# Optimization experiments

Hardware: AMD Instinct MI355X
Metric: run time of the kernel (lower is better)

The kernel has to match this reference:

```python
import jax, jax.numpy as jnp
import numpy as np
from jax import lax

DN = ('NCHW', 'OIHW', 'NCHW')


def conv3x3(x, w, groups=1):
    return lax.conv_general_dilated(x, w, window_strides=(1, 1),
                                    padding=((1, 1), (1, 1)),
                                    dimension_numbers=DN,
                                    feature_group_count=groups)


def conv1x1(x, w):
    return lax.conv_general_dilated(x, w, window_strides=(1, 1),
                                    padding=((0, 0), (0, 0)),
                                    dimension_numbers=DN)


def l2_normalize(t, eps=1e-12):
    n = jnp.sqrt(jnp.sum(t * t, axis=-1, keepdims=True))
    return t / jnp.maximum(n, eps)


def setup_inputs() -> dict:
    key = jax.random.key(0)
    ks = jax.random.split(key, 10)
    B, C, H, W = 4, 64, 256, 256
    heads = 8
    s = 0.05
    return {
        'x': jax.random.normal(ks[0], (B, C, H, W), jnp.float32),
        'w_iem': jax.random.normal(ks[1], (C, C, 3, 3), jnp.float32) * s,
        'w_nem': jax.random.normal(ks[2], (C, C, 3, 3), jnp.float32) * s,
        'w_iem_dw': jax.random.normal(ks[3], (C, 1, 3, 3), jnp.float32) * s,
        'w_nem_dw': jax.random.normal(ks[4], (C, 1, 3, 3), jnp.float32) * s,
        'w_q': jax.random.normal(ks[5], (C, C, 1, 1), jnp.float32) * s,
        'w_k': jax.random.normal(ks[6], (C, C, 1, 1), jnp.float32) * s,
        'w_v': jax.random.normal(ks[7], (C, C, 1, 1), jnp.float32) * s,
        'w_proj': jax.random.normal(ks[8], (C, C, 1, 1), jnp.float32) * s,
        'temperature': jnp.ones((1, heads, 1, 1, 1, 1), jnp.float32),
    }


def igam_forward(x, w_iem, w_nem, w_iem_dw, w_nem_dw, w_q, w_k, w_v, w_proj,
                 temperature, num_heads=8, window_size=8):
    b, c, h, w = x.shape
    ws = window_size
    pad_h = (ws - h % ws) % ws
    pad_w = (ws - w % ws) % ws
    if pad_h or pad_w:  # replicate pad on right/bottom (static)
        x = jnp.pad(x, ((0, 0), (0, 0), (0, pad_h), (0, pad_w)), mode='edge')
    hp, wp = x.shape[-2:]
    heads = num_heads
    d = c // heads
    nh, nw = hp // ws, wp // ws

    illumination_map = conv3x3(jax.nn.sigmoid(conv3x3(x, w_iem)), w_iem_dw, groups=c)
    noise_map = conv3x3(jax.nn.sigmoid(conv3x3(x, w_nem)), w_nem_dw, groups=c)
    illum_scalar = jnp.mean(illumination_map, axis=1, keepdims=True)  # (b,1,hp,wp)
    noise_scalar = jnp.mean(noise_map, axis=1, keepdims=True)

    q = conv1x1(illumination_map, w_q)
    k = conv1x1(noise_map, w_k)
    v = conv1x1(x, w_v)

    def to_windows(t):  # (b,c,hp,wp) -> (b,heads,nh,nw,ws*ws,d)
        t = t.reshape(b, heads, d, hp, wp).transpose(0, 1, 3, 4, 2)
        t = t.reshape(b, heads, nh, ws, nw, ws, d).transpose(0, 1, 2, 4, 3, 5, 6)
        return t.reshape(b, heads, nh, nw, ws * ws, d)

    def scalar_to_windows(t):  # (b,1,hp,wp) -> (b,1,nh,nw,ws*ws,1)
        t = t.reshape(b, 1, nh, ws, nw, ws).transpose(0, 1, 2, 4, 3, 5)
        return t.reshape(b, 1, nh, nw, ws * ws, 1)

    qw = l2_normalize(to_windows(q)) * (1.0 + scalar_to_windows(illum_scalar))
    kw = l2_normalize(to_windows(k)) * jnp.clip(1.0 - scalar_to_windows(noise_scalar), 0.0, 1.0)
    vw = to_windows(v)

    scale = d ** (-0.5)
    attn = jnp.einsum('bhnmqd,bhnmkd->bhnmqk', qw, kw) * scale * temperature
    attn = jax.nn.softmax(attn, axis=-1)
    outw = jnp.einsum('bhnmqk,bhnmkd->bhnmqd', attn, vw)

    # merge windows back to (b, c, hp, wp)
    outw = outw.reshape(b, heads, nh, nw, ws, ws, d).transpose(0, 1, 6, 2, 4, 3, 5)
    out = outw.reshape(b, heads * d, nh * ws, nw * ws)
    if pad_h or pad_w:
        out = out[:, :, :h, :w]
    return conv1x1(out, w_proj)


def reference(x, w_iem, w_nem, w_iem_dw, w_nem_dw, w_q, w_k, w_v, w_proj,
              temperature):
    return igam_forward(x, w_iem, w_nem, w_iem_dw, w_nem_dw, w_q, w_k, w_v,
                        w_proj, temperature)
```

## Files before the change

kernel.cpp:

```cpp
#include <hip/hip_runtime.h>
#include <math.h>

#define W_ 256
#define H_ 256
#define HW 65536
#define CC 64

typedef _Float16 h16;
typedef _Float16 half8 __attribute__((ext_vector_type(8)));
typedef float f32x4  __attribute__((ext_vector_type(4)));
typedef float f32x16 __attribute__((ext_vector_type(16)));

__device__ __forceinline__ unsigned pk2(float a, float b) {
  union { h16 h[2]; unsigned u; } c;
  c.h[0] = (h16)a; c.h[1] = (h16)b;
  return c.u;
}
__device__ __forceinline__ void plswap(unsigned &a, unsigned &b) {
  asm volatile("v_permlane32_swap_b32 %0, %1" : "+v"(a), "+v"(b));
}

__global__ __launch_bounds__(256) void k_wprep(
    const float* __restrict__ wi, const float* __restrict__ wn, h16* __restrict__ Bt)
{
  int i = blockIdx.x * 256 + threadIdx.x;
  if (i >= 128 * 576) return;
  int co = i / 576, k = i - co * 576;
  int tap = k >> 6, ci = k & 63;
  const float* src = (co < 64) ? wi : wn;
  int c = co & 63;
  Bt[i] = (h16)src[(c * 64 + ci) * 9 + tap];
}

__global__ __launch_bounds__(256) void k_wprep2(
    const float* __restrict__ wq, const float* __restrict__ wk,
    const float* __restrict__ wv, const float* __restrict__ wp,
    const float* __restrict__ wdw1, const float* __restrict__ wdw2,
    h16* __restrict__ W)
{
  int i = blockIdx.x * 256 + threadIdx.x;
  if (i >= 17536) return;
  if (i < 16384) {
    int m = i >> 12, e = i & 4095;
    const float* s = (m == 0) ? wq : (m == 1) ? wk : (m == 2) ? wv : wp;
    W[i] = (h16)s[e];
  } else {
    int e = i - 16384;
    int pass = e / 576, rem = e - pass * 576;
    int tap = rem >> 6, c = rem & 63;
    const float* s = pass ? wdw2 : wdw1;
    W[i] = (h16)s[c * 9 + tap];
  }
}

__global__ __launch_bounds__(256) void k_xpose(
    const float* __restrict__ x, h16* __restrict__ xT)
{
  __shared__ __align__(16) char sm[64 * 132];
  const int tid = threadIdx.x;
  const int xt = blockIdx.x, y = blockIdx.y, b = blockIdx.z;
  const int x0 = xt * 64;
  const float* xb = x + ((size_t)b * CC) * HW + y * W_ + x0;
  const int ci = tid >> 2, q = tid & 3;
#pragma unroll
  for (int k = 0; k < 4; ++k) {
    const int pc = q + k * 4;
    float4 v = *(const float4*)(xb + (size_t)ci * HW + pc * 4);
    const int px = pc * 4;
    *(h16*)(sm + (px + 0) * 132 + ci * 2) = (h16)v.x;
    *(h16*)(sm + (px + 1) * 132 + ci * 2) = (h16)v.y;
    *(h16*)(sm + (px + 2) * 132 + ci * 2) = (h16)v.z;
    *(h16*)(sm + (px + 3) * 132 + ci * 2) = (h16)v.w;
  }
  __syncthreads();
  h16* dst = xT + (((size_t)b * 256 + y) * 256 + x0) * 64;
#pragma unroll
  for (int it = 0; it < 2; ++it) {
    int task = tid + it * 256;
    int px = task >> 3, c8 = task & 7;
    int4 d = *(const int4*)(sm + px * 132 + c8 * 16);
    *(int4*)(dst + px * 64 + c8 * 8) = d;
  }
}

__global__ __launch_bounds__(512) void k_conv3x3x2(
    const h16* __restrict__ xT, const h16* __restrict__ Bt,
    h16* __restrict__ T1, h16* __restrict__ T2)
{
  __shared__ __align__(16) char lds[38016];

  const int tid = threadIdx.x;
  const int b = blockIdx.z, ry = blockIdx.y, cx = blockIdx.x;
  const int y0 = ry * 2, x0 = cx * 64;

  {
    const h16* xb = xT + ((size_t)b * 256) * 256 * 64;
    int4 zero4; zero4.x = zero4.y = zero4.z = zero4.w = 0;
#pragma unroll
    for (int it = 0; it < 5; ++it) {
      int idx = tid + it * 512;
      if (idx < 2112) {
        int pxr = idx >> 3, c8 = idx & 7;
        int r = pxr / 66, c = pxr - r * 66;
        int gy = y0 - 1 + r, gx = x0 - 1 + c;
        int4 d = zero4;
        if ((unsigned)gy < 256u && (unsigned)gx < 256u)
          d = *(const int4*)(xb + ((size_t)(gy * 256 + gx)) * 64 + c8 * 8);
        *(int4*)(lds + pxr * 144 + c8 * 16) = d;
      }
    }
  }
  __syncthreads();

  const int wv = tid >> 6, lane = tid & 63;
  const int wn_ = wv & 3;
  const int wm_ = wv >> 2;
  const int cob = wn_ * 32;
  const int pxb = wm_ * 64;
  const int lg = lane >> 4, lr = lane & 15;

  const char* pB[4];
#pragma unroll
  for (int pi = 0; pi < 4; ++pi) {
    int opx = (pxb + pi * 16 + lr) & 63;
    pB[pi] = lds + (wm_ * 66 + opx) * 144 + lg * 16;
  }
  const h16* wb0 = Bt + (size_t)(cob + lr) * 576 + lg * 8;
  const h16* wb1 = wb0 + 16 * 576;

  f32x4 acc[2][4];
#pragma unroll
  for (int i = 0; i < 2; ++i)
#pragma unroll
    for (int j = 0; j < 4; ++j) acc[i][j] = (f32x4){0.f, 0.f, 0.f, 0.f};

#pragma unroll
  for (int tap = 0; tap < 9; ++tap) {
    const int dy = tap / 3, dx = tap - dy * 3;
#pragma unroll
    for (int kh = 0; kh < 2; ++kh) {
      const int loff = (dy * 66 + dx) * 144 + kh * 64;
      const int koff = tap * 64 + kh * 32;
      half8 a0 = *(const half8*)(wb0 + koff);
      half8 a1 = *(const half8*)(wb1 + koff);
      half8 b0 = *(const half8*)(pB[0] + loff);
      half8 b1 = *(const half8*)(pB[1] + loff);
      half8 b2 = *(const half8*)(pB[2] + loff);
      half8 b3 = *(const half8*)(pB[3] + loff);
      acc[0][0] = __builtin_amdgcn_mfma_f32_16x16x32_f16(a0, b0, acc[0][0], 0, 0, 0);
      acc[0][1] = __builtin_amdgcn_mfma_f32_16x16x32_f16(a0, b1, acc[0][1], 0, 0, 0);
      acc[0][2] = __builtin_amdgcn_mfma_f32_16x16x32_f16(a0, b2, acc[0][2], 0, 0, 0);
      acc[0][3] = __builtin_amdgcn_mfma_f32_16x16x32_f16(a0, b3, acc[0][3], 0, 0, 0);
      acc[1][0] = __builtin_amdgcn_mfma_f32_16x16x32_f16(a1, b0, acc[1][0], 0, 0, 0);
      acc[1][1] = __builtin_amdgcn_mfma_f32_16x16x32_f16(a1, b1, acc[1][1], 0, 0, 0);
      acc[1][2] = __builtin_amdgcn_mfma_f32_16x16x32_f16(a1, b2, acc[1][2], 0, 0, 0);
      acc[1][3] = __builtin_amdgcn_mfma_f32_16x16x32_f16(a1, b3, acc[1][3], 0, 0, 0);
    }
  }
  __syncthreads();

#pragma unroll
  for (int ni = 0; ni < 2; ++ni) {
#pragma unroll
    for (int pi = 0; pi < 4; ++pi) {
      const int opx = (pxb + pi * 16 + lr) & 63;
      const int pxid = wm_ * 64 + opx;
      const int co = cob + ni * 16 + lg * 4;
      float s0 = 1.f / (1.f + __expf(-acc[ni][pi][0]));
      float s1 = 1.f / (1.f + __expf(-acc[ni][pi][1]));
      float s2 = 1.f / (1.f + __expf(-acc[ni][pi][2]));
      float s3 = 1.f / (1.f + __expf(-acc[ni][pi][3]));
      uint2 d; d.x = pk2(s0, s1); d.y = pk2(s2, s3);
      *(uint2*)(lds + pxid * 272 + co * 2) = d;
    }
  }
  __syncthreads();

  {
    int px = tid >> 3, chg = tid & 7;
#pragma unroll
    for (int seg = 0; seg < 4; ++seg) {
      int t = seg >> 1, rr = seg & 1;
      int4 d = *(const int4*)(lds + (rr * 64 + px) * 272 + t * 128 + chg * 16);
      h16* dst = (t ? T2 : T1) + (((size_t)b * 256 + (y0 + rr)) * 256 + (x0 + px)) * 64 + chg * 8;
      *(int4*)dst = d;
    }
  }
}

#define HALO 0
#define DWW  14400
#define SIN  16704
#define INA  17216
#define INB  26432
#define INC  35648

__global__ __launch_bounds__(512, 6) void k_megaattn(
    const h16* __restrict__ T1g, const h16* __restrict__ T2g,
    const h16* __restrict__ xT, const h16* __restrict__ Wall,
    const float* __restrict__ temp, float* __restrict__ out)
{
  __shared__ __align__(16) char sm[44864];
  const int tid = threadIdx.x;
  const int wv = tid >> 6, lane = tid & 63;
  const int lg = lane >> 4, lr = lane & 15;
  const int wn = wv & 3;
  const int wm = wv >> 2;

  const int u = blockIdx.x;
  const int xcd = u & 7, idx = u >> 3;
  const int flat = xcd * 512 + idx;
  const int b = flat >> 10, rem = flat & 1023;
  const int wy = rem >> 5, wx = rem & 31;
  const int y0 = wy * 8, x0 = wx * 8;

  half8 wf[4][2];
#pragma unroll
  for (int m = 0; m < 4; ++m)
#pragma unroll
    for (int ks = 0; ks < 2; ++ks)
      wf[m][ks] = *(const half8*)(Wall + m * 4096 + (wn * 16 + lr) * 64 + ks * 32 + lg * 8);
  const float thv = temp[wn * 2 + (lg >> 1)];

  int4 zero4; zero4.x = zero4.y = zero4.z = zero4.w = 0;
  int4 h1r[2], h2r[2], xtr;
#pragma unroll
  for (int i = 0; i < 2; ++i) {
    int cc = tid + i * 512;
    bool act = cc < 800;
    int prow = act ? (cc >> 3) : 0;
    int c8 = cc & 7;
    int hy = prow / 10, hx = prow - hy * 10;
    int gy = y0 - 1 + hy, gx = x0 - 1 + hx;
    bool ok = act && (unsigned)gy < 256u && (unsigned)gx < 256u;
    size_t ga = (((size_t)b * 256 + gy) * 256 + gx) * (size_t)64 + c8 * 8;
    h1r[i] = ok ? *(const int4*)(T1g + ga) : zero4;
    h2r[i] = ok ? *(const int4*)(T2g + ga) : zero4;
  }
  const size_t wbase = (((size_t)b * 256 + y0) * 256 + x0) * 64;
  xtr = *(const int4*)(xT + wbase + (size_t)(tid >> 6) * 16384 + (tid & 63) * 8);

#pragma unroll
  for (int i = 0; i < 2; ++i) {
    int cc = tid + i * 512;
    if (cc < 800) *(int4*)(sm + HALO + (cc >> 3) * 144 + (cc & 7) * 16) = h1r[i];
  }
  {
    int py = tid >> 6, off = tid & 63;
    int px = py * 8 + (off >> 3);
    *(int4*)(sm + INC + px * 144 + (off & 7) * 16) = xtr;
  }
  if (tid < 144) {
    int4 d = *(const int4*)(Wall + 16384 + tid * 8);
    *(int4*)(sm + DWW + tid * 16) = d;
  }
  __syncthreads();

  const half8 hz8 = {(h16)0, (h16)0, (h16)0, (h16)0, (h16)0, (h16)0, (h16)0, (h16)0};
#pragma unroll
  for (int pass = 0; pass < 2; ++pass) {
    const int outb = pass ? INB : INA;
    {
      const int px = tid >> 3, c8 = tid & 7;
      const int py = px >> 3, pxx = px & 7;
      half8 af = hz8;
#pragma unroll
      for (int tap = 0; tap < 9; ++tap) {
        const int dy = tap / 3, dx = tap - dy * 3;
        half8 v  = *(const half8*)(sm + HALO + ((py + dy) * 10 + pxx + dx) * 144 + c8 * 16);
        half8 w8 = *(const half8*)(sm + DWW + pass * 1152 + tap * 128 + c8 * 16);
        af += v * w8;
      }
      *(half8*)(sm + outb + px * 144 + c8 * 16) = af;
    }
    __syncthreads();
    if (pass == 0) {
#pragma unroll
      for (int i = 0; i < 2; ++i) {
        int cc = tid + i * 512;
        if (cc < 800) *(int4*)(sm + HALO + (cc >> 3) * 144 + (cc & 7) * 16) = h2r[i];
      }
      __syncthreads();
    }
  }

  if (tid < 128) {
    int which = tid >> 6, px = tid & 63;
    const char* row = sm + (which ? INB : INA) + px * 144;
    float s = 0.f;
#pragma unroll
    for (int j = 0; j < 8; ++j) {
      half8 v = *(const half8*)(row + j * 16);
#pragma unroll
      for (int e = 0; e < 8; ++e) s += (float)v[e];
    }
    *(float*)(sm + SIN + which * 256 + px * 4) = s * (1.f / 64.f);
  }
  __syncthreads();

  f32x4 aq[2], ak[2], av[2];
#pragma unroll
  for (int pi = 0; pi < 2; ++pi) {
    aq[pi] = (f32x4){0.f, 0.f, 0.f, 0.f};
    ak[pi] = (f32x4){0.f, 0.f, 0.f, 0.f};
    av[pi] = (f32x4){0.f, 0.f, 0.f, 0.f};
  }
  __builtin_amdgcn_s_setprio(1);
#pragma unroll
  for (int pi = 0; pi < 2; ++pi)
#pragma unroll
    for (int ks = 0; ks < 2; ++ks) {
      const int boff = (wm * 32 + pi * 16 + lr) * 144 + ks * 64 + lg * 16;
      half8 b0 = *(const half8*)(sm + INA + boff);
      half8 b1 = *(const half8*)(sm + INB + boff);
      half8 b2 = *(const half8*)(sm + INC + boff);
      aq[pi] = __builtin_amdgcn_mfma_f32_16x16x32_f16(wf[0][ks], b0, aq[pi], 0, 0, 0);
      ak[pi] = __builtin_amdgcn_mfma_f32_16x16x32_f16(wf[1][ks], b1, ak[pi], 0, 0, 0);
      av[pi] = __builtin_amdgcn_mfma_f32_16x16x32_f16(wf[2][ks], b2, av[pi], 0, 0, 0);
    }
  __builtin_amdgcn_s_setprio(0);
  __syncthreads();

#pragma unroll
  for (int pi = 0; pi < 2; ++pi) {
    const int px = wm * 32 + pi * 16 + lr;
    const float si = *(const float*)(sm + SIN + px * 4);
    const float sn = *(const float*)(sm + SIN + 256 + px * 4);
    float s2 = aq[pi][0]*aq[pi][0] + aq[pi][1]*aq[pi][1] + aq[pi][2]*aq[pi][2] + aq[pi][3]*aq[pi][3];
    float qs = (1.f + si) * 0.35355339059327373f * thv /
               fmaxf(sqrtf(s2 + __shfl_xor(s2, 16)), 1e-12f);
    float k2 = ak[pi][0]*ak[pi][0] + ak[pi][1]*ak[pi][1] + ak[pi][2]*ak[pi][2] + ak[pi][3]*ak[pi][3];
    float ks2 = fminf(fmaxf(1.f - sn, 0.f), 1.f) /
                fmaxf(sqrtf(k2 + __shfl_xor(k2, 16)), 1e-12f);
    uint2 dq; dq.x = pk2(aq[pi][0]*qs, aq[pi][1]*qs); dq.y = pk2(aq[pi][2]*qs, aq[pi][3]*qs);
    uint2 dk; dk.x = pk2(ak[pi][0]*ks2, ak[pi][1]*ks2); dk.y = pk2(ak[pi][2]*ks2, ak[pi][3]*ks2);
    *(uint2*)(sm + INA + px * 144 + (wn * 16 + lg * 4) * 2) = dq;
    *(uint2*)(sm + INB + px * 144 + (wn * 16 + lg * 4) * 2) = dk;
#pragma unroll
    for (int r = 0; r < 4; ++r)
      *(h16*)(sm + INC + (wn * 16 + lg * 4 + r) * 144 + px * 2) = (h16)av[pi][r];
  }
  __syncthreads();

  const int l31 = lane & 31, hi = lane >> 5;
  const half8 hz = hz8;
  const f32x16 z16 = {0.f,0.f,0.f,0.f,0.f,0.f,0.f,0.f,0.f,0.f,0.f,0.f,0.f,0.f,0.f,0.f};
  {
    const int h = wv;
    half8 kfr[2], qfr[2];
#pragma unroll
    for (int kt = 0; kt < 2; ++kt)
      kfr[kt] = hi ? hz : *(const half8*)(sm + INB + (kt * 32 + l31) * 144 + h * 16);
#pragma unroll
    for (int qt = 0; qt < 2; ++qt)
      qfr[qt] = hi ? hz : *(const half8*)(sm + INA + (qt * 32 + l31) * 144 + h * 16);

#pragma unroll
    for (int qt = 0; qt < 2; ++qt) {
      __builtin_amdgcn_s_setprio(1);
      f32x16 s0 = __builtin_amdgcn_mfma_f32_32x32x16_f16(kfr[0], qfr[qt], z16, 0, 0, 0);
      f32x16 s1 = __builtin_amdgcn_mfma_f32_32x32x16_f16(kfr[1], qfr[qt], z16, 0, 0, 0);
      __builtin_amdgcn_s_setprio(0);
      float mx = s0[0];
#pragma unroll
      for (int i = 1; i < 16; ++i) mx = fmaxf(mx, s0[i]);
#pragma unroll
      for (int i = 0; i < 16; ++i) mx = fmaxf(mx, s1[i]);
      mx = fmaxf(mx, __shfl_xor(mx, 32));
      float sum = 0.f;
#pragma unroll
      for (int i = 0; i < 16; ++i) { s0[i] = __expf(s0[i] - mx); sum += s0[i]; }
#pragma unroll
      for (int i = 0; i < 16; ++i) { s1[i] = __expf(s1[i] - mx); sum += s1[i]; }
      sum += __shfl_xor(sum, 32);
      const float inv = 1.f / sum;
#pragma unroll
      for (int i = 0; i < 16; ++i) { s0[i] *= inv; s1[i] *= inv; }

      half8 pa[4];
#pragma unroll
      for (int st = 0; st < 4; ++st) {
        const int rb = (st & 1) * 8;
        float p0, p1, p2, p3, p4, p5, p6, p7;
        if (st < 2) {
          p0 = s0[rb+0]; p1 = s0[rb+1]; p2 = s0[rb+2]; p3 = s0[rb+3];
          p4 = s0[rb+4]; p5 = s0[rb+5]; p6 = s0[rb+6]; p7 = s0[rb+7];
        } else {
          p0 = s1[rb+0]; p1 = s1[rb+1]; p2 = s1[rb+2]; p3 = s1[rb+3];
          p4 = s1[rb+4]; p5 = s1[rb+5]; p6 = s1[rb+6]; p7 = s1[rb+7];
        }
        unsigned x0_ = pk2(p0, p1), x1_ = pk2(p2, p3);
        unsigned y0_ = pk2(p4, p5), y1_ = pk2(p6, p7);
        plswap(x0_, y0_);
        plswap(x1_, y1_);
        union { unsigned uu4[4]; half8 h; } uu;
        uu.uu4[0] = x0_; uu.uu4[1] = x1_; uu.uu4[2] = y0_; uu.uu4[3] = y1_;
        pa[st] = uu.h;
      }
      f32x16 oacc = z16;
      __builtin_amdgcn_s_setprio(1);
#pragma unroll
      for (int st = 0; st < 4; ++st) {
        half8 vfr = (l31 < 8)
          ? *(const half8*)(sm + INC + (h * 8 + l31) * 144 + (st * 16 + hi * 8) * 2)
          : hz;
        oacc = __builtin_amdgcn_mfma_f32_32x32x16_f16(pa[st], vfr, oacc, 0, 0, 0);
      }
      __builtin_amdgcn_s_setprio(0);
      if (l31 < 8) {
#pragma unroll
        for (int r = 0; r < 16; ++r) {
          const int q = qt * 32 + (r & 3) + 8 * (r >> 2) + 4 * hi;
          *(h16*)(sm + INA + q * 144 + (h * 8 + l31) * 2) = (h16)oacc[r];
        }
      }
    }
  }
  __syncthreads();

  f32x4 pacc[2];
#pragma unroll
  for (int pi = 0; pi < 2; ++pi) pacc[pi] = (f32x4){0.f, 0.f, 0.f, 0.f};
  __builtin_amdgcn_s_setprio(1);
#pragma unroll
  for (int pi = 0; pi < 2; ++pi)
#pragma unroll
    for (int ks = 0; ks < 2; ++ks) {
      half8 bfr = *(const half8*)(sm + INA + (wm * 32 + pi * 16 + lr) * 144 + ks * 64 + lg * 16);
      pacc[pi] = __builtin_amdgcn_mfma_f32_16x16x32_f16(wf[3][ks], bfr, pacc[pi], 0, 0, 0);
    }
  __builtin_amdgcn_s_setprio(0);
#pragma unroll
  for (int pi = 0; pi < 2; ++pi) {
    const int px = wm * 32 + pi * 16 + lr;
    const int py = px >> 3, pxx = px & 7;
    const int co = wn * 16 + lg * 4;
    float* ob = out + ((size_t)(b * CC + co)) * HW + (size_t)(y0 + py) * W_ + (x0 + pxx);
    ob[0]      = pacc[pi][0];
    ob[HW]     = pacc[pi][1];
    ob[2 * HW] = pacc[pi][2];
    ob[3 * HW] = pacc[pi][3];
  }
}

extern "C" void kernel_launch(void* const* d_in, const int* in_sizes, int n_in,
                              void* d_out, int out_size, void* d_ws, size_t ws_size,
                              hipStream_t stream) {
  const float* x        = (const float*)d_in[0];
  const float* w_iem    = (const float*)d_in[1];
  const float* w_nem    = (const float*)d_in[2];
  const float* w_iem_dw = (const float*)d_in[3];
  const float* w_nem_dw = (const float*)d_in[4];
  const float* w_q      = (const float*)d_in[5];
  const float* w_k      = (const float*)d_in[6];
  const float* w_v      = (const float*)d_in[7];
  const float* w_proj   = (const float*)d_in[8];
  const float* temp     = (const float*)d_in[9];
  float* outp = (float*)d_out;

  const size_t PLE = (size_t)4 * CC * HW;
  h16* h0   = (h16*)d_ws;
  h16* T1   = h0;
  h16* T2   = h0 + PLE;
  h16* xT   = h0 + 2 * PLE;
  h16* Bt   = h0 + 3 * PLE;
  h16* Wall = Bt + 73728;

  dim3 b256(256), b512(512);

  k_wprep    <<<dim3(288),        b256, 0, stream>>>(w_iem, w_nem, Bt);
  k_wprep2   <<<dim3(69),         b256, 0, stream>>>(w_q, w_k, w_v, w_proj,
                                                     w_iem_dw, w_nem_dw, Wall);
  k_xpose    <<<dim3(4, 256, 4),  b256, 0, stream>>>(x, xT);
  k_conv3x3x2<<<dim3(4, 128, 4),  b512, 0, stream>>>(xT, Bt, T1, T2);
  k_megaattn <<<dim3(4096),       b512, 0, stream>>>(T1, T2, xT, Wall, temp, outp);
}
```

Measured before the change: 204.8 us.

## Streamline window softmax and fuse channel-mean into depthwise pass

Computes the per-pixel channel mean inside the depthwise-conv pass using wave shuffles, which removes a separate LDS re-read stage. The softmax drops max subtraction, since the L2-normalized q and k keep the logits bounded. The log2(e) factor is folded into the q scale so the kernel can use the native exp2. Normalization by the row sum is deferred to the PV output, and the PV MFMA operands are swapped so each lane writes one packed 4-element store. Skipping the max relies on the logits staying small, which costs some numerical robustness if the illumination scalar or temperature grows large.

```diff
diff --git a/kernel.cpp b/kernel.cpp
--- a/kernel.cpp
+++ b/kernel.cpp
@@ -245,11 +245,6 @@
     int cc = tid + i * 512;
     if (cc < 800) *(int4*)(sm + HALO + (cc >> 3) * 144 + (cc & 7) * 16) = h1r[i];
   }
-  {
-    int py = tid >> 6, off = tid & 63;
-    int px = py * 8 + (off >> 3);
-    *(int4*)(sm + INC + px * 144 + (off & 7) * 16) = xtr;
-  }
   if (tid < 144) {
     int4 d = *(const int4*)(Wall + 16384 + tid * 8);
     *(int4*)(sm + DWW + tid * 16) = d;
@@ -272,6 +267,13 @@
         af += v * w8;
       }
       *(half8*)(sm + outb + px * 144 + c8 * 16) = af;
+      float s = 0.f;
+#pragma unroll
+      for (int j = 0; j < 8; ++j) s += (float)af[j];
+      s += __shfl_xor(s, 1);
+      s += __shfl_xor(s, 2);
+      s += __shfl_xor(s, 4);
+      if (c8 == 0) *(float*)(sm + SIN + pass * 256 + px * 4) = s * (1.f / 64.f);
     }
     __syncthreads();
     if (pass == 0) {
@@ -284,17 +286,10 @@
     }
   }
 
-  if (tid < 128) {
-    int which = tid >> 6, px = tid & 63;
-    const char* row = sm + (which ? INB : INA) + px * 144;
-    float s = 0.f;
-#pragma unroll
-    for (int j = 0; j < 8; ++j) {
-      half8 v = *(const half8*)(row + j * 16);
-#pragma unroll
-      for (int e = 0; e < 8; ++e) s += (float)v[e];
-    }
-    *(float*)(sm + SIN + which * 256 + px * 4) = s * (1.f / 64.f);
+  {
+    int py = tid >> 6, off = tid & 63;
+    int px = py * 8 + (off >> 3);
+    *(int4*)(sm + INC + px * 144 + (off & 7) * 16) = xtr;
   }
   __syncthreads();
 
@@ -327,7 +322,7 @@
     const float si = *(const float*)(sm + SIN + px * 4);
     const float sn = *(const float*)(sm + SIN + 256 + px * 4);
     float s2 = aq[pi][0]*aq[pi][0] + aq[pi][1]*aq[pi][1] + aq[pi][2]*aq[pi][2] + aq[pi][3]*aq[pi][3];
-    float qs = (1.f + si) * 0.35355339059327373f * thv /
+    float qs = (1.f + si) * (0.35355339059327373f * 1.4426950408889634f) * thv /
                fmaxf(sqrtf(s2 + __shfl_xor(s2, 16)), 1e-12f);
     float k2 = ak[pi][0]*ak[pi][0] + ak[pi][1]*ak[pi][1] + ak[pi][2]*ak[pi][2] + ak[pi][3]*ak[pi][3];
     float ks2 = fminf(fmaxf(1.f - sn, 0.f), 1.f) /
@@ -361,21 +356,13 @@
       f32x16 s0 = __builtin_amdgcn_mfma_f32_32x32x16_f16(kfr[0], qfr[qt], z16, 0, 0, 0);
       f32x16 s1 = __builtin_amdgcn_mfma_f32_32x32x16_f16(kfr[1], qfr[qt], z16, 0, 0, 0);
       __builtin_amdgcn_s_setprio(0);
-      float mx = s0[0];
-#pragma unroll
-      for (int i = 1; i < 16; ++i) mx = fmaxf(mx, s0[i]);
-#pragma unroll
-      for (int i = 0; i < 16; ++i) mx = fmaxf(mx, s1[i]);
-      mx = fmaxf(mx, __shfl_xor(mx, 32));
       float sum = 0.f;
 #pragma unroll
-      for (int i = 0; i < 16; ++i) { s0[i] = __expf(s0[i] - mx); sum += s0[i]; }
-#pragma unroll
-      for (int i = 0; i < 16; ++i) { s1[i] = __expf(s1[i] - mx); sum += s1[i]; }
+      for (int i = 0; i < 16; ++i) { s0[i] = __builtin_amdgcn_exp2f(s0[i]); sum += s0[i]; }
+#pragma unroll
+      for (int i = 0; i < 16; ++i) { s1[i] = __builtin_amdgcn_exp2f(s1[i]); sum += s1[i]; }
       sum += __shfl_xor(sum, 32);
       const float inv = 1.f / sum;
-#pragma unroll
-      for (int i = 0; i < 16; ++i) { s0[i] *= inv; s1[i] *= inv; }
 
       half8 pa[4];
 #pragma unroll
@@ -404,15 +391,14 @@
         half8 vfr = (l31 < 8)
           ? *(const half8*)(sm + INC + (h * 8 + l31) * 144 + (st * 16 + hi * 8) * 2)
           : hz;
-        oacc = __builtin_amdgcn_mfma_f32_32x32x16_f16(pa[st], vfr, oacc, 0, 0, 0);
+        oacc = __builtin_amdgcn_mfma_f32_32x32x16_f16(vfr, pa[st], oacc, 0, 0, 0);
       }
       __builtin_amdgcn_s_setprio(0);
-      if (l31 < 8) {
-#pragma unroll
-        for (int r = 0; r < 16; ++r) {
-          const int q = qt * 32 + (r & 3) + 8 * (r >> 2) + 4 * hi;
-          *(h16*)(sm + INA + q * 144 + (h * 8 + l31) * 2) = (h16)oacc[r];
-        }
+      {
+        uint2 dAO;
+        dAO.x = pk2(oacc[0] * inv, oacc[1] * inv);
+        dAO.y = pk2(oacc[2] * inv, oacc[3] * inv);
+        *(uint2*)(sm + INA + (qt * 32 + l31) * 144 + (h * 8 + 4 * hi) * 2) = dAO;
       }
     }
   }
```

Measured after the change: 192.1 us (median of 2 runs). 6.2% less time.
